# Optimization experiments

Hardware: AMD Instinct MI355X
Metric: run time of the kernel (lower is better)

Reference implementation:

```python
import jax, jax.numpy as jnp
import numpy as np

NUM_LAYERS = 4
EPS = 1e-8


def setup_inputs() -> dict:
    key = jax.random.key(0)
    ks = jax.random.split(key, 7)
    N, D, H = 8192, 1024, 4096
    return {
        "x": jax.random.normal(ks[0], (N, D), jnp.float32),
        "fc1_W": jax.random.normal(ks[1], (H, D), jnp.float32) * 0.02,
        "fc1_b": jax.random.normal(ks[2], (H,), jnp.float32) * 0.02,
        "fc2_W": jax.random.normal(ks[3], (D, H), jnp.float32) * 0.02,
        "fc2_b": jax.random.normal(ks[4], (D,), jnp.float32) * 0.02,
        "comp_W": jax.random.normal(ks[5], (NUM_LAYERS + 1, D, D), jnp.float32) * 0.03,
        "comp_b": jax.random.normal(ks[6], (NUM_LAYERS + 1, D), jnp.float32) * 0.03,
    }


def _block(x, fc1_W, fc1_b, fc2_W, fc2_b):
    # fc2(dropout(fc1(x))) in eval mode; relu is defined but never applied
    h = x @ fc1_W.T + fc1_b
    return h @ fc2_W.T + fc2_b


def _compute_loss(z, W, b):
    # out = Linear(z); per-row cosine_similarity(out_i.unsqueeze(1), out_i.unsqueeze(0))
    # reduces broadcast dim 1 -> vector c[j] = out[j]*sum(out) / max(|out[j]|*sqrt(y)*||out||, eps)
    # which torch broadcasts into constant rows of a [y,y] matrix; the
    # abs-diff accumulation over batch rows is then rank-1.
    out = z @ W.T + b                                # [N, y]
    y = out.shape[-1]
    S = out.sum(-1, keepdims=True)                   # [N, 1]
    n2 = jnp.sqrt((out * out).sum(-1, keepdims=True))  # [N, 1] row norms
    n1 = jnp.abs(out) * jnp.sqrt(jnp.asarray(y, out.dtype))  # [N, y]
    c = out * S / jnp.maximum(n1 * n2, EPS)          # [N, y]
    D = jnp.abs(c[1:] - c[:-1]).sum(0)               # [y]
    return jnp.broadcast_to(D, (y, y))               # [y, y]


def reference(x, fc1_W, fc1_b, fc2_W, fc2_b, comp_W, comp_b):
    inv = _block(x, fc1_W, fc1_b, fc2_W, fc2_b)
    loss = _compute_loss(inv, comp_W[0], comp_b[0])
    nxt = x - inv
    inv_total = inv
    for i in range(1, NUM_LAYERS + 1):
        inv_new = _block(nxt, fc1_W, fc1_b, fc2_W, fc2_b)
        inv_total = inv_total + inv_new
        loss = loss + _compute_loss(inv_new, comp_W[i], comp_b[i])
        nxt = nxt - inv_new
    return inv_total, nxt, loss
```

## Files before the change

### kernel.cpp

```cpp
#include <hip/hip_runtime.h>
#include <hip/hip_bf16.h>


#define NR 8192
#define DD 1024
#define HH 4096
#define NL 5
#define MSZ (DD * DD)

using bf16 = __hip_bfloat16;
typedef __attribute__((ext_vector_type(8))) short bf16x8;
typedef __attribute__((ext_vector_type(4))) float f32x4;


__global__ void cvt_bf16_kernel(const float* __restrict__ in, bf16* __restrict__ out, int n4) {
  int i = blockIdx.x * 256 + threadIdx.x;
  int stride = gridDim.x * 256;
  union U { bf16 b[4]; uint2 u; };
  for (; i < n4; i += stride) {
    float4 v = ((const float4*)in)[i];
    U u;
    u.b[0] = __float2bfloat16(v.x); u.b[1] = __float2bfloat16(v.y);
    u.b[2] = __float2bfloat16(v.z); u.b[3] = __float2bfloat16(v.w);
    ((uint2*)out)[i] = u.u;
  }
}

__global__ void transpose_cvt_kernel(const float* __restrict__ in, bf16* __restrict__ out) {
  __shared__ bf16 tile[64][74];
  int c0 = blockIdx.x * 64;
  int r0 = blockIdx.y * 64;
  int col = threadIdx.x & 63;
  int row4 = threadIdx.x >> 6;
  #pragma unroll
  for (int j = 0; j < 16; ++j) {
    int r = row4 * 16 + j;
    tile[r][col] = __float2bfloat16(in[(size_t)(r0 + r) * DD + c0 + col]);
  }
  __syncthreads();
  #pragma unroll
  for (int j = 0; j < 16; ++j) {
    int r = row4 * 16 + j;
    out[(size_t)(c0 + r) * HH + r0 + col] = tile[col][r];
  }
}

__global__ void cvec_kernel(const float* __restrict__ fc1_b, const float* __restrict__ fc2_W,
                            const float* __restrict__ fc2_b, float* __restrict__ c) {
  int j = blockIdx.x;
  float s = 0.f;
  for (int k = threadIdx.x; k < HH; k += 256) s += fc1_b[k] * fc2_W[(size_t)j * HH + k];
  for (int o = 32; o; o >>= 1) s += __shfl_down(s, o);
  __shared__ float red[4];
  if ((threadIdx.x & 63) == 0) red[threadIdx.x >> 6] = s;
  __syncthreads();
  if (threadIdx.x == 0) c[j] = red[0] + red[1] + red[2] + red[3] + fc2_b[j];
}

__global__ void zero_kernel(float* __restrict__ p, int n) {
  int i = blockIdx.x * 256 + threadIdx.x;
  if (i < n) p[i] = 0.f;
}

__global__ void mbuild_kernel(const float* __restrict__ Cp,
                              bf16* __restrict__ M, bf16* __restrict__ Mt,
                              bf16* __restrict__ T, bf16* __restrict__ Tt) {
  __shared__ float tile[64][65];
  int n0 = blockIdx.x * 64, m0 = blockIdx.y * 64;
  int tn = threadIdx.x & 63, tm4 = threadIdx.x >> 6;
  #pragma unroll
  for (int j = 0; j < 16; ++j) {
    int m = tm4 * 16 + j;
    size_t idx = (size_t)(m0 + m) * DD + n0 + tn;
    float v = Cp[idx] + Cp[MSZ + idx] + Cp[2 * MSZ + idx] + Cp[3 * MSZ + idx];
    tile[m][tn] = v;
    float d = ((m0 + m) == (n0 + tn)) ? 1.f : 0.f;
    M[idx] = __float2bfloat16(v);
    T[idx] = __float2bfloat16(d - v);
  }
  __syncthreads();
  #pragma unroll
  for (int j = 0; j < 16; ++j) {
    int r = tm4 * 16 + j;
    float v = tile[tn][r];
    size_t idx = (size_t)(n0 + r) * DD + m0 + tn;
    float d = ((n0 + r) == (m0 + tn)) ? 1.f : 0.f;
    Mt[idx] = __float2bfloat16(v);
    Tt[idx] = __float2bfloat16(d - v);
  }
}

__global__ void sbuild_kernel(const bf16* __restrict__ Pw, bf16* __restrict__ S) {
  int idx = blockIdx.x * 256 + threadIdx.x;
  int m = idx >> 10, n = idx & (DD - 1);
  float v = (m == n) ? 1.f : 0.f;
  v += __bfloat162float(Pw[idx]) + __bfloat162float(Pw[MSZ + idx])
     + __bfloat162float(Pw[2 * MSZ + idx]) + __bfloat162float(Pw[3 * MSZ + idx]);
  S[idx] = __float2bfloat16(v);
}

__global__ void vecmat_kernel(const float* __restrict__ v, const bf16* __restrict__ Bt,
                              float* __restrict__ out) {
  int z = blockIdx.y, j = blockIdx.x;
  const bf16* row = Bt + (size_t)z * MSZ + (size_t)j * DD;
  float s = 0.f;
  for (int k = threadIdx.x; k < DD; k += 256) s += v[k] * __bfloat162float(row[k]);
  for (int o = 32; o; o >>= 1) s += __shfl_down(s, o);
  __shared__ float red[4];
  if ((threadIdx.x & 63) == 0) red[threadIdx.x >> 6] = s;
  __syncthreads();
  if (threadIdx.x == 0) out[(size_t)z * DD + j] = red[0] + red[1] + red[2] + red[3];
}

__global__ void biasall_kernel(const float* __restrict__ cvec, const float* __restrict__ ebuf,
                               const float* __restrict__ comp_W, const float* __restrict__ comp_b,
                               float* __restrict__ biasall) {
  int z = blockIdx.y, j = blockIdx.x;
  if (z == 0) {
    if (threadIdx.x == 0)
      biasall[j] = cvec[j] + ebuf[j] + ebuf[DD + j] + ebuf[2 * DD + j] + ebuf[3 * DD + j];
    return;
  }
  int i = z - 1;
  const float* e = (i == 0) ? cvec : ebuf + (size_t)(i - 1) * DD;
  const float* wr = comp_W + (size_t)i * MSZ + (size_t)j * DD;
  float s = 0.f;
  for (int k = threadIdx.x; k < DD; k += 256) s += e[k] * wr[k];
  for (int o = 32; o; o >>= 1) s += __shfl_down(s, o);
  __shared__ float red[4];
  if ((threadIdx.x & 63) == 0) red[threadIdx.x >> 6] = s;
  __syncthreads();
  if (threadIdx.x == 0)
    biasall[(size_t)z * DD + j] = red[0] + red[1] + red[2] + red[3] + comp_b[(size_t)i * DD + j];
}


__device__ __forceinline__ void async16(const bf16* g, bf16* l) {
  __builtin_amdgcn_global_load_lds(
      (const __attribute__((address_space(1))) void*)g,
      (__attribute__((address_space(3))) void*)l, 16, 0, 0);
}

__device__ __forceinline__ void gemm_core_async(
    const bf16* __restrict__ A, const bf16* __restrict__ B,
    int kBeg, int kEnd, int lda, int ldb, int bm, int bn,
    bf16* As, bf16* Bs, f32x4 acc[4][4])
{
  const int tid  = threadIdx.x;
  const int lane = tid & 63;
  const int wave = tid >> 6;
  const int wm = (wave & 1) * 64;
  const int wn = (wave >> 1) * 64;
  const int lr = lane >> 3;
  const int lcol = ((lane & 7) ^ lr) * 8;
  const bf16* gA = A + (size_t)(bm + wave * 32 + lr) * lda + lcol;
  const bf16* gB = B + (size_t)(bn + wave * 32 + lr) * ldb + lcol;
  bf16* lA = As + wave * 32 * 64;
  bf16* lB = Bs + wave * 32 * 64;

  for (int k0 = kBeg; k0 < kEnd; k0 += 64) {
    #pragma unroll
    for (int it = 0; it < 4; ++it) {
      async16(gA + (size_t)(it * 8) * lda + k0, lA + it * 8 * 64);
      async16(gB + (size_t)(it * 8) * ldb + k0, lB + it * 8 * 64);
    }
    __syncthreads();
    #pragma unroll
    for (int ks = 0; ks < 2; ++ks) {
      bf16x8 av[4], bv[4];
      #pragma unroll
      for (int i = 0; i < 4; ++i) {
        const int rr = i * 16 + (lane & 15);
        const int cc = ((ks * 4 + (lane >> 4)) ^ (lane & 7)) * 8;
        av[i] = *(const bf16x8*)(As + (wm + rr) * 64 + cc);
        bv[i] = *(const bf16x8*)(Bs + (wn + rr) * 64 + cc);
      }
      #pragma unroll
      for (int i = 0; i < 4; ++i)
        #pragma unroll
        for (int j = 0; j < 4; ++j)
          acc[i][j] = __builtin_amdgcn_mfma_f32_16x16x32_bf16(av[i], bv[j], acc[i][j], 0, 0, 0);
    }
    __syncthreads();
  }
}

#define GEMM_PROLOGUE \
  alignas(16) __shared__ bf16 As[128 * 64]; \
  alignas(16) __shared__ bf16 Bs[128 * 64]; \
  f32x4 acc[4][4] = {}; \
  const int lane = threadIdx.x & 63; \
  const int wm = ((threadIdx.x >> 6) & 1) * 64; \
  const int wn = ((threadIdx.x >> 6) >> 1) * 64;

__global__ __launch_bounds__(256, 2)
void gemm_splitk(const bf16* __restrict__ A, const bf16* __restrict__ B, float* __restrict__ Cp) {
  GEMM_PROLOGUE
  const int bm = blockIdx.y * 128, bn = blockIdx.x * 128;
  const int kb = blockIdx.z * (HH / 4);
  gemm_core_async(A, B, kb, kb + HH / 4, HH, HH, bm, bn, As, Bs, acc);
  float* C = Cp + (size_t)blockIdx.z * MSZ;
  #pragma unroll
  for (int i = 0; i < 4; ++i)
    #pragma unroll
    for (int j = 0; j < 4; ++j) {
      const int col = bn + wn + j * 16 + (lane & 15);
      #pragma unroll
      for (int r = 0; r < 4; ++r) {
        const int row = bm + wm + i * 16 + (lane >> 4) * 4 + r;
        C[(size_t)row * DD + col] = acc[i][j][r];
      }
    }
}

__global__ __launch_bounds__(256, 2)
void gemm_dual(const bf16* __restrict__ A, const bf16* __restrict__ B,
               bf16* __restrict__ Ct, bf16* __restrict__ Cn) {
  GEMM_PROLOGUE
  const int bm = blockIdx.y * 128, bn = blockIdx.x * 128;
  gemm_core_async(A, B, 0, DD, DD, DD, bm, bn, As, Bs, acc);
  #pragma unroll
  for (int i = 0; i < 4; ++i)
    #pragma unroll
    for (int j = 0; j < 4; ++j) {
      const int col = bn + wn + j * 16 + (lane & 15);
      const int row0 = bm + wm + i * 16 + (lane >> 4) * 4;
      union { bf16 b[4]; uint2 u; } pk;
      #pragma unroll
      for (int r = 0; r < 4; ++r) {
        bf16 v = __float2bfloat16(acc[i][j][r]);
        pk.b[r] = v;
        Cn[(size_t)(row0 + r) * DD + col] = v;
      }
      *(uint2*)(&Ct[(size_t)col * DD + row0]) = pk.u;
    }
}

__global__ __launch_bounds__(256, 2)
void gemm_b4(const bf16* __restrict__ A0, long astr, const bf16* __restrict__ B0, long bstr,
             bf16* __restrict__ C0, long cstr,
             const bf16* __restrict__ A2, const bf16* __restrict__ B2, bf16* __restrict__ C2,
             int zswitch) {
  GEMM_PROLOGUE
  const int z = blockIdx.z;
  const bf16* A; const bf16* B; bf16* C;
  if (z < zswitch) { A = A0 + (size_t)z * astr; B = B0 + (size_t)z * bstr; C = C0 + (size_t)z * cstr; }
  else             { A = A2; B = B2; C = C2; }
  const int bm = blockIdx.y * 128, bn = blockIdx.x * 128;
  gemm_core_async(A, B, 0, DD, DD, DD, bm, bn, As, Bs, acc);
  #pragma unroll
  for (int i = 0; i < 4; ++i)
    #pragma unroll
    for (int j = 0; j < 4; ++j) {
      const int col = bn + wn + j * 16 + (lane & 15);
      #pragma unroll
      for (int r = 0; r < 4; ++r) {
        const int row = bm + wm + i * 16 + (lane >> 4) * 4 + r;
        C[(size_t)row * DD + col] = __float2bfloat16(acc[i][j][r]);
      }
    }
}

__global__ __launch_bounds__(256, 2)
void gemm_main(const bf16* __restrict__ A, const bf16* __restrict__ Bb,
               const float* __restrict__ biasall, const float* __restrict__ x,
               float* __restrict__ invtot, float* __restrict__ nxtf,
               unsigned long long* __restrict__ sgn,
               float* __restrict__ Srow, float* __restrict__ Qrow) {
  GEMM_PROLOGUE
  const int bm = blockIdx.y * 128, bn = blockIdx.x * 128;
  gemm_core_async(A, Bb + (size_t)(bn >> 10) * MSZ, 0, DD, DD, DD, bm, bn & (DD - 1), As, Bs, acc);

  if (bn < DD) {
    #pragma unroll
    for (int i = 0; i < 4; ++i)
      #pragma unroll
      for (int j = 0; j < 4; ++j) {
        const int col = bn + wn + j * 16 + (lane & 15);
        const float bj = biasall[col];
        #pragma unroll
        for (int r = 0; r < 4; ++r) {
          const int row = bm + wm + i * 16 + (lane >> 4) * 4 + r;
          const float v = acc[i][j][r] + bj;
          const size_t idx = (size_t)row * DD + col;
          invtot[idx] = v;
          nxtf[idx] = x[idx] - v;
        }
      }
  } else {
    const int z = (bn >> 10) - 1;
    const int rb = bm >> 7;
    const int cb = (bn & (DD - 1)) >> 7;
    const int wave = threadIdx.x >> 6;
    unsigned long long keep = 0ULL;
    float sv[4][4] = {}, qv[4][4] = {};
    #pragma unroll
    for (int i = 0; i < 4; ++i)
      #pragma unroll
      for (int j = 0; j < 4; ++j) {
        const int colg = bn + wn + j * 16 + (lane & 15);
        const float bj = biasall[colg];
        #pragma unroll
        for (int r = 0; r < 4; ++r) {
          const float v = acc[i][j][r] + bj;
          const unsigned long long bal = __ballot(v < 0.f);
          if (lane == i * 16 + j * 4 + r) keep = bal;
          sv[i][r] += v;
          qv[i][r] += v * v;
        }
      }
    const size_t wbase = ((((size_t)z * 64 + rb) * 8 + cb) * 4 + wave) * 64;
    sgn[wbase + lane] = keep;
    #pragma unroll
    for (int i = 0; i < 4; ++i)
      #pragma unroll
      for (int r = 0; r < 4; ++r) {
        float s = sv[i][r], q = qv[i][r];
        #pragma unroll
        for (int off = 1; off < 16; off <<= 1) { s += __shfl_xor(s, off); q += __shfl_xor(q, off); }
        if ((lane & 15) == 0) {
          const int row = bm + wm + i * 16 + (lane >> 4) * 4 + r;
          atomicAdd(&Srow[(size_t)z * NR + row], s);
          atomicAdd(&Qrow[(size_t)z * NR + row], q);
        }
      }
  }
}


__global__ void losssign_kernel(const unsigned long long* __restrict__ sgn,
                                const float* __restrict__ Srow, const float* __restrict__ Qrow,
                                float* __restrict__ Dtot) {
  const int z = blockIdx.y;
  const int cg = blockIdx.x;
  const int n0 = blockIdx.z * 1024;
  __shared__ float rsh[1025];
  const float* S = Srow + (size_t)z * NR;
  const float* Q = Qrow + (size_t)z * NR;
  for (int t = threadIdx.x; t < 1025; t += 256) {
    int n = n0 + t; if (n > NR - 1) n = NR - 1;
    rsh[t] = S[n] * rsqrtf(Q[n]) * 0.03125f;
  }
  __syncthreads();
  const int c = threadIdx.x & 63;
  const int q = threadIdx.x >> 6;
  const int col = cg * 64 + c;
  const int cb = col >> 7;
  const int wsel = (col >> 6) & 1;
  const int jf = (col >> 4) & 3;
  const int c15 = col & 15;
  const size_t zbase = (size_t)z * 64 * 8 * 4 * 64;
  const int ns = n0 + q * 256;
  int ne = ns + 256; if (ne > NR - 1) ne = NR - 1;

  auto cval = [&](int n) -> float {
    const int rbk = n >> 7, nl = n & 127;
    const int wave = (nl >> 6) | (wsel << 1);
    const int i = (nl >> 4) & 3, rg = (nl >> 2) & 3, r = nl & 3;
    const size_t widx = zbase + ((((size_t)rbk * 8 + cb) * 4 + wave) * 64)
                      + i * 16 + jf * 4 + r;
    const unsigned long long wv = sgn[widx];
    const float rv = rsh[n - n0];
    return ((wv >> (rg * 16 + c15)) & 1ULL) ? -rv : rv;
  };

  float d = 0.f;
  float cprev = cval(ns);
  for (int n = ns + 1; n <= ne; ++n) {
    const float cn = cval(n);
    d += fabsf(cn - cprev);
    cprev = cn;
  }
  atomicAdd(&Dtot[z * DD + col], d);
}

__global__ void writeloss_kernel(const float* __restrict__ Dtot, float* __restrict__ out) {
  int idx = blockIdx.x * 256 + threadIdx.x;
  int j = idx & (DD - 1);
  out[idx] = Dtot[j] + Dtot[DD + j] + Dtot[2 * DD + j] + Dtot[3 * DD + j] + Dtot[4 * DD + j];
}


extern "C" void kernel_launch(void* const* d_in, const int* in_sizes, int n_in,
                              void* d_out, int out_size, void* d_ws, size_t ws_size,
                              hipStream_t stream) {
  const float* x      = (const float*)d_in[0];
  const float* fc1_W  = (const float*)d_in[1];
  const float* fc1_b  = (const float*)d_in[2];
  const float* fc2_W  = (const float*)d_in[3];
  const float* fc2_b  = (const float*)d_in[4];
  const float* comp_W = (const float*)d_in[5];
  const float* comp_b = (const float*)d_in[6];

  float* invtot  = (float*)d_out;
  float* nxtf    = invtot + (size_t)NR * DD;
  float* lossout = invtot + (size_t)2 * NR * DD;

  char* w = (char*)d_ws;
  auto alloc = [&](size_t bytes) { char* p = w; w += (bytes + 255) & ~(size_t)255; return p; };
  bf16* x_bf     = (bf16*)alloc((size_t)NR * DD * 2);
  bf16* fc1T_bf  = (bf16*)alloc((size_t)DD * HH * 2);
  bf16* fc2_bf   = (bf16*)alloc((size_t)DD * HH * 2);
  bf16* compW_bf = (bf16*)alloc((size_t)NL * MSZ * 2);
  bf16* M_bf     = (bf16*)alloc((size_t)MSZ * 2);
  bf16* Mt_bf    = (bf16*)alloc((size_t)MSZ * 2);
  bf16* Tt_buf   = (bf16*)alloc((size_t)2 * MSZ * 2);
  bf16* Pw       = (bf16*)alloc((size_t)4 * MSZ * 2);
  bf16* S_bf     = (bf16*)alloc((size_t)MSZ * 2);
  bf16* Gt       = (bf16*)alloc((size_t)NL * MSZ * 2);
  bf16* Bbig     = (bf16*)alloc((size_t)6 * MSZ * 2);
  unsigned long long* sgn = (unsigned long long*)alloc((size_t)NL * 64 * 8 * 4 * 64 * 8);
  float* Cp      = (float*)alloc((size_t)4 * MSZ * 4);
  float* cvec    = (float*)alloc(DD * 4);
  float* ebuf    = (float*)alloc((size_t)4 * DD * 4);
  float* biasall = (float*)alloc((size_t)6 * DD * 4);
  float* stats   = (float*)alloc((size_t)(NL * DD + 2 * NL * NR) * 4);
  float* Dtot = stats;
  float* Srow = stats + NL * DD;
  float* Qrow = Srow + (size_t)NL * NR;
  (void)ws_size; (void)in_sizes; (void)n_in; (void)out_size;

  cvt_bf16_kernel<<<2048, 256, 0, stream>>>(x, x_bf, NR * DD / 4);
  cvt_bf16_kernel<<<1024, 256, 0, stream>>>(fc2_W, fc2_bf, DD * HH / 4);
  cvt_bf16_kernel<<<1024, 256, 0, stream>>>(comp_W, compW_bf, NL * MSZ / 4);
  transpose_cvt_kernel<<<dim3(DD / 64, HH / 64), 256, 0, stream>>>(fc1_W, fc1T_bf);
  cvec_kernel<<<DD, 256, 0, stream>>>(fc1_b, fc2_W, fc2_b, cvec);
  zero_kernel<<<(NL * DD + 2 * NL * NR + 255) / 256, 256, 0, stream>>>(stats, NL * DD + 2 * NL * NR);

  gemm_splitk<<<dim3(8, 8, 4), 256, 0, stream>>>(fc1T_bf, fc2_bf, Cp);
  mbuild_kernel<<<dim3(16, 16), 256, 0, stream>>>(Cp, M_bf, Mt_bf, Pw, Tt_buf);
  gemm_b4<<<dim3(8, 8, NL), 256, 0, stream>>>(compW_bf, MSZ, M_bf, 0, Gt, MSZ,
                                              nullptr, nullptr, nullptr, 99);
  hipMemcpyAsync(Bbig + MSZ, Gt, (size_t)MSZ * 2, hipMemcpyDeviceToDevice, stream);
  gemm_dual<<<dim3(8, 8), 256, 0, stream>>>(Pw, Tt_buf, Tt_buf + MSZ, Pw + MSZ);
  gemm_b4<<<dim3(8, 8, 2), 256, 0, stream>>>(Pw + MSZ, 0, Tt_buf, MSZ, Pw + 2 * MSZ, MSZ,
                                             nullptr, nullptr, nullptr, 99);
  sbuild_kernel<<<MSZ / 256, 256, 0, stream>>>(Pw, S_bf);
  gemm_b4<<<dim3(8, 8, NL), 256, 0, stream>>>(Gt + MSZ, MSZ, Pw, MSZ, Bbig + 2 * MSZ, MSZ,
                                              Mt_bf, S_bf, Bbig, 4);
  vecmat_kernel<<<dim3(DD, 2), 256, 0, stream>>>(cvec, Tt_buf, ebuf);
  vecmat_kernel<<<dim3(DD, 2), 256, 0, stream>>>(ebuf + DD, Tt_buf, ebuf + 2 * DD);
  biasall_kernel<<<dim3(DD, 6), 256, 0, stream>>>(cvec, ebuf, comp_W, comp_b, biasall);

  gemm_main<<<dim3(6 * DD / 128, NR / 128), 256, 0, stream>>>(
      x_bf, Bbig, biasall, x, invtot, nxtf, sgn, Srow, Qrow);

  losssign_kernel<<<dim3(16, NL, 8), 256, 0, stream>>>(sgn, Srow, Qrow, Dtot);
  writeloss_kernel<<<MSZ / 256, 256, 0, stream>>>(Dtot, lossout);
}
```

Measured before the change: 513.2 us.

## Restructure weight-composition precompute with differenced power matrices and fused prep kernel

```diff
diff --git a/kernel.cpp b/kernel.cpp
--- a/kernel.cpp
+++ b/kernel.cpp
@@ -13,16 +13,35 @@
 typedef __attribute__((ext_vector_type(4))) float f32x4;
 
 
-__global__ void cvt_bf16_kernel(const float* __restrict__ in, bf16* __restrict__ out, int n4) {
+__device__ __forceinline__ void cvt4(const float* __restrict__ in, bf16* __restrict__ out, int i) {
+  float4 v = ((const float4*)in)[i];
+  union { bf16 b[4]; uint2 u; } u;
+  u.b[0] = __float2bfloat16(v.x); u.b[1] = __float2bfloat16(v.y);
+  u.b[2] = __float2bfloat16(v.z); u.b[3] = __float2bfloat16(v.w);
+  ((uint2*)out)[i] = u.u;
+}
+
+#define NX4 (NR * DD / 4)
+#define NF4 (DD * HH / 4)
+#define NC4 (NL * MSZ / 4)
+#define NS4 ((NL * DD + 2 * NL * NR) / 4)
+#define NE4 (DD)
+
+__global__ void prep_kernel(const float* __restrict__ x, const float* __restrict__ fc2_W,
+                            const float* __restrict__ comp_W,
+                            bf16* __restrict__ x_bf, bf16* __restrict__ fc2_bf,
+                            bf16* __restrict__ compW_bf,
+                            float* __restrict__ stats, float* __restrict__ ebuf) {
   int i = blockIdx.x * 256 + threadIdx.x;
-  int stride = gridDim.x * 256;
-  union U { bf16 b[4]; uint2 u; };
-  for (; i < n4; i += stride) {
-    float4 v = ((const float4*)in)[i];
-    U u;
-    u.b[0] = __float2bfloat16(v.x); u.b[1] = __float2bfloat16(v.y);
-    u.b[2] = __float2bfloat16(v.z); u.b[3] = __float2bfloat16(v.w);
-    ((uint2*)out)[i] = u.u;
+  const int stride = gridDim.x * 256;
+  const int total = NX4 + NF4 + NC4 + NS4 + NE4;
+  const float4 z4 = {0.f, 0.f, 0.f, 0.f};
+  for (; i < total; i += stride) {
+    if (i < NX4) cvt4(x, x_bf, i);
+    else if (i < NX4 + NF4) cvt4(fc2_W, fc2_bf, i - NX4);
+    else if (i < NX4 + NF4 + NC4) cvt4(comp_W, compW_bf, i - NX4 - NF4);
+    else if (i < NX4 + NF4 + NC4 + NS4) ((float4*)stats)[i - NX4 - NF4 - NC4] = z4;
+    else ((float4*)ebuf)[i - NX4 - NF4 - NC4 - NS4] = z4;
   }
 }
 
@@ -57,14 +76,8 @@
   if (threadIdx.x == 0) c[j] = red[0] + red[1] + red[2] + red[3] + fc2_b[j];
 }
 
-__global__ void zero_kernel(float* __restrict__ p, int n) {
-  int i = blockIdx.x * 256 + threadIdx.x;
-  if (i < n) p[i] = 0.f;
-}
-
 __global__ void mbuild_kernel(const float* __restrict__ Cp,
-                              bf16* __restrict__ M, bf16* __restrict__ Mt,
-                              bf16* __restrict__ T, bf16* __restrict__ Tt) {
+                              bf16* __restrict__ M, bf16* __restrict__ T, bf16* __restrict__ Tt) {
   __shared__ float tile[64][65];
   int n0 = blockIdx.x * 64, m0 = blockIdx.y * 64;
   int tn = threadIdx.x & 63, tm4 = threadIdx.x >> 6;
@@ -85,31 +98,20 @@
     float v = tile[tn][r];
     size_t idx = (size_t)(n0 + r) * DD + m0 + tn;
     float d = ((n0 + r) == (m0 + tn)) ? 1.f : 0.f;
-    Mt[idx] = __float2bfloat16(v);
     Tt[idx] = __float2bfloat16(d - v);
   }
 }
 
-__global__ void sbuild_kernel(const bf16* __restrict__ Pw, bf16* __restrict__ S) {
-  int idx = blockIdx.x * 256 + threadIdx.x;
-  int m = idx >> 10, n = idx & (DD - 1);
-  float v = (m == n) ? 1.f : 0.f;
-  v += __bfloat162float(Pw[idx]) + __bfloat162float(Pw[MSZ + idx])
-     + __bfloat162float(Pw[2 * MSZ + idx]) + __bfloat162float(Pw[3 * MSZ + idx]);
-  S[idx] = __float2bfloat16(v);
-}
-
-__global__ void vecmat_kernel(const float* __restrict__ v, const bf16* __restrict__ Bt,
-                              float* __restrict__ out) {
-  int z = blockIdx.y, j = blockIdx.x;
-  const bf16* row = Bt + (size_t)z * MSZ + (size_t)j * DD;
+__global__ void gemv4_kernel(const float* __restrict__ c, const bf16* __restrict__ Pw,
+                             float* __restrict__ ebuf) {
+  const int z = blockIdx.y;
+  const int j = blockIdx.x * 256 + threadIdx.x;
+  const bf16* P = Pw + (size_t)z * MSZ + j;
+  const int k0 = blockIdx.z * 256;
   float s = 0.f;
-  for (int k = threadIdx.x; k < DD; k += 256) s += v[k] * __bfloat162float(row[k]);
-  for (int o = 32; o; o >>= 1) s += __shfl_down(s, o);
-  __shared__ float red[4];
-  if ((threadIdx.x & 63) == 0) red[threadIdx.x >> 6] = s;
-  __syncthreads();
-  if (threadIdx.x == 0) out[(size_t)z * DD + j] = red[0] + red[1] + red[2] + red[3];
+  #pragma unroll 8
+  for (int k = k0; k < k0 + 256; ++k) s += c[k] * __bfloat162float(P[(size_t)k * DD]);
+  atomicAdd(&ebuf[z * DD + j], s);
 }
 
 __global__ void biasall_kernel(const float* __restrict__ cvec, const float* __restrict__ ebuf,
@@ -262,8 +264,39 @@
 }
 
 __global__ __launch_bounds__(256, 2)
+void gemm_t5(const bf16* __restrict__ A, const bf16* __restrict__ B,
+             const bf16* __restrict__ Pw, bf16* __restrict__ Dl, bf16* __restrict__ Bbig0) {
+  GEMM_PROLOGUE
+  const int bm = blockIdx.y * 128, bn = blockIdx.x * 128;
+  gemm_core_async(A, B, 0, DD, DD, DD, bm, bn, As, Bs, acc);
+  #pragma unroll
+  for (int i = 0; i < 4; ++i)
+    #pragma unroll
+    for (int j = 0; j < 4; ++j) {
+      const int col = bn + wn + j * 16 + (lane & 15);
+      const int row0 = bm + wm + i * 16 + (lane >> 4) * 4;
+      union { bf16 b[4]; uint2 u; } pk;
+      #pragma unroll
+      for (int r = 0; r < 4; ++r) {
+        const size_t idx = (size_t)(row0 + r) * DD + col;
+        const float t1 = __bfloat162float(Pw[idx]);
+        const float t2 = __bfloat162float(Pw[MSZ + idx]);
+        const float t3 = __bfloat162float(Pw[2 * MSZ + idx]);
+        const float t4 = __bfloat162float(Pw[3 * MSZ + idx]);
+        const float t5 = acc[i][j][r];
+        Dl[idx]           = __float2bfloat16(t1 - t2);
+        Dl[MSZ + idx]     = __float2bfloat16(t2 - t3);
+        Dl[2 * MSZ + idx] = __float2bfloat16(t3 - t4);
+        Dl[3 * MSZ + idx] = __float2bfloat16(t4 - t5);
+        pk.b[r] = __float2bfloat16((((row0 + r) == col) ? 1.f : 0.f) - t5);
+      }
+      *(uint2*)(&Bbig0[(size_t)col * DD + row0]) = pk.u;
+    }
+}
+
+__global__ __launch_bounds__(256, 2)
 void gemm_main(const bf16* __restrict__ A, const bf16* __restrict__ Bb,
-               const float* __restrict__ biasall, const float* __restrict__ x,
+               const float* __restrict__ biasall, const bf16* __restrict__ xb,
                float* __restrict__ invtot, float* __restrict__ nxtf,
                unsigned long long* __restrict__ sgn,
                float* __restrict__ Srow, float* __restrict__ Qrow) {
@@ -284,7 +317,7 @@
           const float v = acc[i][j][r] + bj;
           const size_t idx = (size_t)row * DD + col;
           invtot[idx] = v;
-          nxtf[idx] = x[idx] - v;
+          nxtf[idx] = __bfloat162float(xb[idx]) - v;
         }
       }
   } else {
@@ -402,12 +435,11 @@
   bf16* fc1T_bf  = (bf16*)alloc((size_t)DD * HH * 2);
   bf16* fc2_bf   = (bf16*)alloc((size_t)DD * HH * 2);
   bf16* compW_bf = (bf16*)alloc((size_t)NL * MSZ * 2);
-  bf16* M_bf     = (bf16*)alloc((size_t)MSZ * 2);
-  bf16* Mt_bf    = (bf16*)alloc((size_t)MSZ * 2);
+  bf16* Dbank    = (bf16*)alloc((size_t)5 * MSZ * 2);
+  bf16* M_bf = Dbank;
+  bf16* Dl   = Dbank + MSZ;
   bf16* Tt_buf   = (bf16*)alloc((size_t)2 * MSZ * 2);
   bf16* Pw       = (bf16*)alloc((size_t)4 * MSZ * 2);
-  bf16* S_bf     = (bf16*)alloc((size_t)MSZ * 2);
-  bf16* Gt       = (bf16*)alloc((size_t)NL * MSZ * 2);
   bf16* Bbig     = (bf16*)alloc((size_t)6 * MSZ * 2);
   unsigned long long* sgn = (unsigned long long*)alloc((size_t)NL * 64 * 8 * 4 * 64 * 8);
   float* Cp      = (float*)alloc((size_t)4 * MSZ * 4);
@@ -420,30 +452,23 @@
   float* Qrow = Srow + (size_t)NL * NR;
   (void)ws_size; (void)in_sizes; (void)n_in; (void)out_size;
 
-  cvt_bf16_kernel<<<2048, 256, 0, stream>>>(x, x_bf, NR * DD / 4);
-  cvt_bf16_kernel<<<1024, 256, 0, stream>>>(fc2_W, fc2_bf, DD * HH / 4);
-  cvt_bf16_kernel<<<1024, 256, 0, stream>>>(comp_W, compW_bf, NL * MSZ / 4);
+  prep_kernel<<<2048, 256, 0, stream>>>(x, fc2_W, comp_W, x_bf, fc2_bf, compW_bf, stats, ebuf);
   transpose_cvt_kernel<<<dim3(DD / 64, HH / 64), 256, 0, stream>>>(fc1_W, fc1T_bf);
   cvec_kernel<<<DD, 256, 0, stream>>>(fc1_b, fc2_W, fc2_b, cvec);
-  zero_kernel<<<(NL * DD + 2 * NL * NR + 255) / 256, 256, 0, stream>>>(stats, NL * DD + 2 * NL * NR);
 
   gemm_splitk<<<dim3(8, 8, 4), 256, 0, stream>>>(fc1T_bf, fc2_bf, Cp);
-  mbuild_kernel<<<dim3(16, 16), 256, 0, stream>>>(Cp, M_bf, Mt_bf, Pw, Tt_buf);
-  gemm_b4<<<dim3(8, 8, NL), 256, 0, stream>>>(compW_bf, MSZ, M_bf, 0, Gt, MSZ,
-                                              nullptr, nullptr, nullptr, 99);
-  hipMemcpyAsync(Bbig + MSZ, Gt, (size_t)MSZ * 2, hipMemcpyDeviceToDevice, stream);
+  mbuild_kernel<<<dim3(16, 16), 256, 0, stream>>>(Cp, M_bf, Pw, Tt_buf);
   gemm_dual<<<dim3(8, 8), 256, 0, stream>>>(Pw, Tt_buf, Tt_buf + MSZ, Pw + MSZ);
   gemm_b4<<<dim3(8, 8, 2), 256, 0, stream>>>(Pw + MSZ, 0, Tt_buf, MSZ, Pw + 2 * MSZ, MSZ,
                                              nullptr, nullptr, nullptr, 99);
-  sbuild_kernel<<<MSZ / 256, 256, 0, stream>>>(Pw, S_bf);
-  gemm_b4<<<dim3(8, 8, NL), 256, 0, stream>>>(Gt + MSZ, MSZ, Pw, MSZ, Bbig + 2 * MSZ, MSZ,
-                                              Mt_bf, S_bf, Bbig, 4);
-  vecmat_kernel<<<dim3(DD, 2), 256, 0, stream>>>(cvec, Tt_buf, ebuf);
-  vecmat_kernel<<<dim3(DD, 2), 256, 0, stream>>>(ebuf + DD, Tt_buf, ebuf + 2 * DD);
+  gemm_t5<<<dim3(8, 8), 256, 0, stream>>>(Pw + 3 * MSZ, Tt_buf, Pw, Dl, Bbig);
+  gemv4_kernel<<<dim3(4, 4, 4), 256, 0, stream>>>(cvec, Pw, ebuf);
   biasall_kernel<<<dim3(DD, 6), 256, 0, stream>>>(cvec, ebuf, comp_W, comp_b, biasall);
+  gemm_b4<<<dim3(8, 8, NL), 256, 0, stream>>>(compW_bf, MSZ, Dbank, MSZ, Bbig + MSZ, MSZ,
+                                              nullptr, nullptr, nullptr, 99);
 
   gemm_main<<<dim3(6 * DD / 128, NR / 128), 256, 0, stream>>>(
-      x_bf, Bbig, biasall, x, invtot, nxtf, sgn, Srow, Qrow);
+      x_bf, Bbig, biasall, x_bf, invtot, nxtf, sgn, Srow, Qrow);
 
   losssign_kernel<<<dim3(16, NL, 8), 256, 0, stream>>>(sgn, Srow, Qrow, Dtot);
   writeloss_kernel<<<MSZ / 256, 256, 0, stream>>>(Dtot, lossout);
```

New measurement: 514.7 us. About the same (+0.3%).
